# Kernel optimization log

Hardware: AMD Instinct MI355X
Metric: run time of the kernel (lower is better)

Reference implementation:

```python
import jax, jax.numpy as jnp
import numpy as np

N_HEAD = 12

def setup_inputs() -> dict:
    key = jax.random.key(0)
    ks = jax.random.split(key, 5)
    B, T, C = 4, 2048, 768
    x = jax.random.normal(ks[0], (B, T, C), dtype=jnp.float32)
    s_in = 1.0 / np.sqrt(C)
    W_qkv = jax.random.normal(ks[1], (C, 3 * C), dtype=jnp.float32) * s_in
    b_qkv = jnp.zeros((3 * C,), dtype=jnp.float32)
    W_proj = jax.random.normal(ks[2], (C, C), dtype=jnp.float32) * s_in
    b_proj = jnp.zeros((C,), dtype=jnp.float32)
    return {"x": x, "W_qkv": W_qkv, "b_qkv": b_qkv, "W_proj": W_proj, "b_proj": b_proj}


def reference(x, W_qkv, b_qkv, W_proj, b_proj):
    B, T, C = x.shape
    H = N_HEAD
    D = C // H  # head dim
    qkv = x @ W_qkv + b_qkv                      # [B,T,3C]
    q, k, v = jnp.split(qkv, 3, axis=-1)
    # [B,T,C] -> [B,H,T,D]
    q = q.reshape(B, T, H, D).transpose(0, 2, 1, 3)
    k = k.reshape(B, T, H, D).transpose(0, 2, 1, 3)
    v = v.reshape(B, T, H, D).transpose(0, 2, 1, 3)
    att = jnp.einsum("bhqd,bhkd->bhqk", q, k) / jnp.sqrt(jnp.asarray(D, x.dtype))
    causal = jnp.tril(jnp.ones((T, T), dtype=bool))
    att = jnp.where(causal, att, jnp.asarray(-jnp.inf, att.dtype))
    att = jax.nn.softmax(att, axis=-1)
    y = jnp.einsum("bhqk,bhkd->bhqd", att, v)    # [B,H,T,D]
    y = y.transpose(0, 2, 1, 3).reshape(B, T, C)
    return y @ W_proj + b_proj
```

## Files before the change

### kernel.cpp

```cpp
#include <hip/hip_runtime.h>
#include <hip/hip_bf16.h>

typedef __bf16 bf16x8 __attribute__((ext_vector_type(8)));
typedef float f32x4 __attribute__((ext_vector_type(4)));
typedef unsigned int u32x4 __attribute__((ext_vector_type(4)));
typedef unsigned int u32x2 __attribute__((ext_vector_type(2)));
typedef int i32x2 __attribute__((ext_vector_type(2)));
typedef unsigned short u16;
typedef unsigned long long u64;

#define WAITVM(n) asm volatile("s_waitcnt vmcnt(" #n ")" ::: "memory")
#define SBAR() asm volatile("s_barrier" ::: "memory")

__device__ __forceinline__ u16 f2bf(float f) {
  unsigned u = __builtin_bit_cast(unsigned, f);
  u += 0x7FFFu + ((u >> 16) & 1u);
  return (u16)(u >> 16);
}
__device__ __forceinline__ unsigned cvtpk(float a, float b) {
  float2 f; f.x = a; f.y = b;
  __hip_bfloat162 h = __float22bfloat162_rn(f);
  unsigned u;
  __builtin_memcpy(&u, &h, 4);
  return u;
}

__device__ __forceinline__ void plswap(unsigned &a, unsigned &b) {
  i32x2 r = __builtin_amdgcn_permlane32_swap((int)a, (int)b, false, false);
  a = (unsigned)r[0];
  b = (unsigned)r[1];
}

__device__ __forceinline__ void gll16(const u16* g, u16* l) {
  __builtin_amdgcn_global_load_lds(
      (const __attribute__((address_space(1))) unsigned int*)g,
      (__attribute__((address_space(3))) unsigned int*)l, 16, 0, 0);
}

__global__ void cast_x_kernel(const float* __restrict__ in, u16* __restrict__ out, int n4) {
  int i = blockIdx.x * blockDim.x + threadIdx.x;
  if (i >= n4) return;
  f32x4 v = *(const f32x4*)(in + (size_t)i * 4);
  u32x2 pk;
  pk[0] = cvtpk(v[0], v[1]);
  pk[1] = cvtpk(v[2], v[3]);
  *(u32x2*)(out + (size_t)i * 4) = pk;
}

__global__ void transpose_cast_kernel(const float* __restrict__ W, u16* __restrict__ WT, int K, int N) {
  __shared__ float tile[32][33];
  int c0 = blockIdx.x * 32, r0 = blockIdx.y * 32;
  int tx = threadIdx.x & 31, tg = threadIdx.x >> 5;
#pragma unroll
  for (int i = 0; i < 4; ++i) {
    int r = tg + i * 8;
    tile[r][tx] = W[(size_t)(r0 + r) * N + c0 + tx];
  }
  __syncthreads();
#pragma unroll
  for (int i = 0; i < 4; ++i) {
    int r = tg + i * 8;
    WT[(size_t)(c0 + r) * K + r0 + tx] = f2bf(tile[tx][r]);
  }
}

__global__ __launch_bounds__(256, 3) void gemm_qkv_kernel(
    const u16* __restrict__ A, const u16* __restrict__ BT, const float* __restrict__ bias,
    u16* __restrict__ Qb, u16* __restrict__ Kb, u16* __restrict__ Vt) {
  constexpr int K = 768;
  constexpr int NS = K / 32;
  __shared__ u16 Asm[3][128 * 32];
  __shared__ u16 Bsm[3][128 * 32];
  const int tid = threadIdx.x;
  const int w = tid >> 6, lane = tid & 63;
  const int l15 = lane & 15, quad = lane >> 4;
  const int srow = tid >> 2, scol = (tid & 3) * 8;
  const int m0 = blockIdx.y * 128, n0 = blockIdx.x * 128;
  const u16* Ag = A + (size_t)(m0 + srow) * K + scol;
  const u16* Bg = BT + (size_t)(n0 + srow) * K + scol;
  const int mw = (w >> 1) * 64, nw = (w & 1) * 64;
  f32x4 acc[4][4];
#pragma unroll
  for (int i = 0; i < 4; ++i)
#pragma unroll
    for (int j = 0; j < 4; ++j) acc[i][j] = {0.f, 0.f, 0.f, 0.f};

  auto STAGE = [&](int buf, int ks) {
    const u16* a = Ag + ks * 32;
    const u16* b = Bg + ks * 32;
#pragma unroll
    for (int rb = 0; rb < 2; ++rb) {
      gll16(a + (size_t)rb * 64 * K, &Asm[buf][(rb * 64 + w * 16) * 32]);
      gll16(b + (size_t)rb * 64 * K, &Bsm[buf][(rb * 64 + w * 16) * 32]);
    }
  };
  auto COMPUTE = [&](int buf) {
    bf16x8 af[4], bfj[4];
#pragma unroll
    for (int i = 0; i < 4; ++i) af[i] = *(const bf16x8*)&Asm[buf][(mw + i * 16 + l15) * 32 + quad * 8];
#pragma unroll
    for (int j = 0; j < 4; ++j) bfj[j] = *(const bf16x8*)&Bsm[buf][(nw + j * 16 + l15) * 32 + quad * 8];
#pragma unroll
    for (int i = 0; i < 4; ++i)
#pragma unroll
      for (int j = 0; j < 4; ++j)
        acc[i][j] = __builtin_amdgcn_mfma_f32_16x16x32_bf16(af[i], bfj[j], acc[i][j], 0, 0, 0);
  };

  STAGE(0, 0);
  STAGE(1, 1);
  for (int s = 0; s < NS - 3; s += 3) {
    STAGE((s + 2) % 3, s + 2); WAITVM(8); SBAR(); COMPUTE(s % 3); SBAR();
    STAGE((s + 3) % 3, s + 3); WAITVM(8); SBAR(); COMPUTE((s + 1) % 3); SBAR();
    STAGE((s + 4) % 3, s + 4); WAITVM(8); SBAR(); COMPUTE((s + 2) % 3); SBAR();
  }
  STAGE((NS - 1) % 3, NS - 1); WAITVM(8); SBAR(); COMPUTE((NS - 3) % 3); SBAR();
  WAITVM(4); SBAR(); COMPUTE((NS - 2) % 3); SBAR();
  WAITVM(0); SBAR(); COMPUTE((NS - 1) % 3);

  const int sec = blockIdx.x / 6;
  const int nbase = n0 - sec * 768;
#pragma unroll
  for (int j = 0; j < 4; ++j) {
    const int nloc = nbase + nw + j * 16 + l15;
    const float bv = bias[sec * 768 + nloc];
    const int h = nloc >> 6, d = nloc & 63;
#pragma unroll
    for (int i = 0; i < 4; ++i) {
      const int m = m0 + mw + i * 16 + quad * 4;
      const int bb = m >> 11, trow = m & 2047;
      if (sec == 2) {
        u32x2 pk;
        pk[0] = cvtpk(acc[i][j][0] + bv, acc[i][j][1] + bv);
        pk[1] = cvtpk(acc[i][j][2] + bv, acc[i][j][3] + bv);
        *(u32x2*)(Vt + (size_t)((bb * 12 + h) * 64 + d) * 2048 + trow) = pk;
      } else {
        u16* dst = (sec == 0) ? Qb : Kb;
        const float scl = (sec == 0) ? 0.125f * 1.44269504f : 1.0f;
#pragma unroll
        for (int r = 0; r < 4; ++r)
          dst[(size_t)((bb * 12 + h) * 2048 + trow + r) * 64 + d] = f2bf((acc[i][j][r] + bv) * scl);
      }
    }
  }
}

__global__ __launch_bounds__(256, 4) void gemm_proj_kernel(
    const u16* __restrict__ A, const u16* __restrict__ BT, const float* __restrict__ bias,
    float* __restrict__ out) {
  constexpr int K = 768;
  constexpr int NS = K / 32;
  __shared__ u16 Asm[2][64 * 32];
  __shared__ u16 Bsm[2][128 * 32];
  const int lin = blockIdx.y * 6 + blockIdx.x;
  const int swz = (lin & 7) * 96 + (lin >> 3);
  const int tid = threadIdx.x;
  const int w = tid >> 6, lane = tid & 63;
  const int l15 = lane & 15, quad = lane >> 4;
  const int srow = tid >> 2, scol = (tid & 3) * 8;
  const int m0 = (swz / 6) * 64, n0 = (swz % 6) * 128;
  const u16* Ag = A + (size_t)(m0 + srow) * K + scol;
  const u16* Bg = BT + (size_t)(n0 + srow) * K + scol;
  const int mw = (w >> 1) * 32, nw = (w & 1) * 64;
  f32x4 acc[2][4];
#pragma unroll
  for (int i = 0; i < 2; ++i)
#pragma unroll
    for (int j = 0; j < 4; ++j) acc[i][j] = {0.f, 0.f, 0.f, 0.f};

  auto STAGE = [&](int buf, int ks) {
    const u16* a = Ag + ks * 32;
    const u16* b = Bg + ks * 32;
    gll16(a, &Asm[buf][(w * 16) * 32]);
#pragma unroll
    for (int rb = 0; rb < 2; ++rb)
      gll16(b + (size_t)rb * 64 * K, &Bsm[buf][(rb * 64 + w * 16) * 32]);
  };
  auto COMPUTE = [&](int buf) {
    bf16x8 af[2], bfj[4];
#pragma unroll
    for (int i = 0; i < 2; ++i) af[i] = *(const bf16x8*)&Asm[buf][(mw + i * 16 + l15) * 32 + quad * 8];
#pragma unroll
    for (int j = 0; j < 4; ++j) bfj[j] = *(const bf16x8*)&Bsm[buf][(nw + j * 16 + l15) * 32 + quad * 8];
#pragma unroll
    for (int i = 0; i < 2; ++i)
#pragma unroll
      for (int j = 0; j < 4; ++j)
        acc[i][j] = __builtin_amdgcn_mfma_f32_16x16x32_bf16(af[i], bfj[j], acc[i][j], 0, 0, 0);
  };

  STAGE(0, 0);
  WAITVM(0); SBAR();
  for (int s = 0; s < NS; ++s) {
    const int buf = s & 1;
    if (s + 1 < NS) STAGE(buf ^ 1, s + 1);
    COMPUTE(buf);
    WAITVM(0); SBAR();
  }

#pragma unroll
  for (int j = 0; j < 4; ++j) {
    const int n = n0 + nw + j * 16 + l15;
    const float bv = bias[n];
#pragma unroll
    for (int i = 0; i < 2; ++i) {
      const int m = m0 + mw + i * 16 + quad * 4;
#pragma unroll
      for (int r = 0; r < 4; ++r) out[(size_t)(m + r) * 768 + n] = acc[i][j][r] + bv;
    }
  }
}

__global__ __launch_bounds__(512) void attn_split_kernel(
    const u16* __restrict__ Qg, const u16* __restrict__ Kg, const u16* __restrict__ Vtg,
    u16* __restrict__ Yb, float* __restrict__ Opart, float* __restrict__ lpart) {
  constexpr int T = 2048, D = 64;
  constexpr int LDP = 72;
  constexpr float MBOUND = 20.0f;
  __shared__ u16 Ks[2][64 * LDP];
  __shared__ u16 VTs[2][64 * LDP];
  const int lin = blockIdx.y * 40 + blockIdx.x;
  const int swzb = (lin & 7) * 240 + (lin >> 3);
  const int s = 39 - (swzb % 40);
  const int bh = swzb / 40;
  int qt2, c;
  if (s < 4) { qt2 = s; c = 0; }
  else if (s < 12) { qt2 = 4 + ((s - 4) >> 1); c = (s - 4) & 1; }
  else if (s < 24) { int u = s - 12; int q3 = u / 3; qt2 = 8 + q3; c = u - 3 * q3; }
  else { int u = s - 24; qt2 = 12 + (u >> 2); c = u & 3; }
  const int nkt = 2 * qt2 + 2;
  const int niter = min(8, nkt - 8 * c);
  const int tid = threadIdx.x;
  const int w = tid >> 6, lane = tid & 63;
  const int l15 = lane & 15, quad = lane >> 4;
  const int srow = tid >> 3;
  const int scol = (tid & 7) * 8;
  const int so0 = scol - 4 * (tid & 1);
  const int so1 = scol + 8 - 4 * (tid & 1);
  const u16* Kp = Kg + (size_t)bh * T * D;
  const u16* VTp = Vtg + (size_t)bh * D * T;

  const int wdiag = 2 * qt2 + (w >> 2);
  const int qq = qt2 * 128 + w * 16 + l15;
  const u16* qrow = Qg + ((size_t)bh * T + qq) * D;
  const bf16x8 qfa = *(const bf16x8*)(qrow + quad * 8);
  const bf16x8 qfb = *(const bf16x8*)(qrow + 32 + quad * 8);

  u32x4 onesw; onesw[0] = 0x3F803F80u; onesw[1] = 0x3F803F80u; onesw[2] = 0x3F803F80u; onesw[3] = 0x3F803F80u;
  const bf16x8 ones = __builtin_bit_cast(bf16x8, onesw);

  f32x4 o[4] = {{0,0,0,0},{0,0,0,0},{0,0,0,0},{0,0,0,0}};
  f32x4 lacc = {0.f, 0.f, 0.f, 0.f};

  u32x4 kA, vA;
  auto LOADT = [&](int kt) {
    const int k1 = kt * 64;
    kA = *(const u32x4*)(Kp + (size_t)(k1 + srow) * D + scol);
    vA = *(const u32x4*)(VTp + (size_t)srow * T + k1 + scol);
  };
  auto STORET = [&](int buf) {
    *(u32x4*)&Ks[buf][srow * LDP + scol] = kA;
    u32x2 vlo; vlo[0] = vA[0]; vlo[1] = vA[1];
    u32x2 vhi; vhi[0] = vA[2]; vhi[1] = vA[3];
    *(u32x2*)&VTs[buf][srow * LDP + so0] = vlo;
    *(u32x2*)&VTs[buf][srow * LDP + so1] = vhi;
  };

  LOADT(c * 8);
  STORET(0);
  if (niter > 1) LOADT(c * 8 + 1);
  __syncthreads();

  for (int j = 0; j < niter; ++j) {
    const int buf = j & 1;
    const int ktg = c * 8 + j;
    if (ktg <= wdiag) {
      f32x4 sA[4];
#pragma unroll
      for (int t = 0; t < 4; ++t) sA[t] = {-MBOUND, -MBOUND, -MBOUND, -MBOUND};
      __builtin_amdgcn_s_setprio(1);
#pragma unroll
      for (int t = 0; t < 4; ++t) {
        const bf16x8 kf0 = *(const bf16x8*)&Ks[buf][(t * 16 + l15) * LDP + quad * 8];
        const bf16x8 kf1 = *(const bf16x8*)&Ks[buf][(t * 16 + l15) * LDP + 32 + quad * 8];
        sA[t] = __builtin_amdgcn_mfma_f32_16x16x32_bf16(kf0, qfa, sA[t], 0, 0, 0);
        sA[t] = __builtin_amdgcn_mfma_f32_16x16x32_bf16(kf1, qfb, sA[t], 0, 0, 0);
      }
      __builtin_amdgcn_s_setprio(0);
      if (ktg == wdiag) {
        const int k0 = ktg * 64;
#pragma unroll
        for (int t = 0; t < 4; ++t)
#pragma unroll
          for (int r = 0; r < 4; ++r)
            if (k0 + t * 16 + quad * 4 + r > qq) sA[t][r] = -1e30f;
      }
      unsigned W[4][2];
#pragma unroll
      for (int t = 0; t < 4; ++t) {
        float e0 = __builtin_amdgcn_exp2f(sA[t][0]);
        float e1 = __builtin_amdgcn_exp2f(sA[t][1]);
        float e2 = __builtin_amdgcn_exp2f(sA[t][2]);
        float e3 = __builtin_amdgcn_exp2f(sA[t][3]);
        W[t][0] = cvtpk(e0, e1);
        W[t][1] = cvtpk(e2, e3);
      }
      plswap(W[0][0], W[1][0]);
      plswap(W[0][1], W[1][1]);
      plswap(W[2][0], W[3][0]);
      plswap(W[2][1], W[3][1]);
      u32x4 paw; paw[0] = W[0][0]; paw[1] = W[0][1]; paw[2] = W[1][0]; paw[3] = W[1][1];
      u32x4 pbw; pbw[0] = W[2][0]; pbw[1] = W[2][1]; pbw[2] = W[3][0]; pbw[3] = W[3][1];
      const bf16x8 pa = __builtin_bit_cast(bf16x8, paw);
      const bf16x8 pb = __builtin_bit_cast(bf16x8, pbw);
      __builtin_amdgcn_s_setprio(1);
      lacc = __builtin_amdgcn_mfma_f32_16x16x32_bf16(ones, pa, lacc, 0, 0, 0);
      lacc = __builtin_amdgcn_mfma_f32_16x16x32_bf16(ones, pb, lacc, 0, 0, 0);
#pragma unroll
      for (int t = 0; t < 4; ++t) {
        const bf16x8 vf0 = *(const bf16x8*)&VTs[buf][(t * 16 + l15) * LDP + quad * 8];
        const bf16x8 vf1 = *(const bf16x8*)&VTs[buf][(t * 16 + l15) * LDP + 32 + quad * 8];
        o[t] = __builtin_amdgcn_mfma_f32_16x16x32_bf16(vf0, pa, o[t], 0, 0, 0);
        o[t] = __builtin_amdgcn_mfma_f32_16x16x32_bf16(vf1, pb, o[t], 0, 0, 0);
      }
      __builtin_amdgcn_s_setprio(0);
    }
    if (j + 1 < niter) {
      STORET(buf ^ 1);
      if (j + 2 < niter) LOADT(c * 8 + j + 2);
    }
    __syncthreads();
  }

  const float lv = lacc[0];
  if (qt2 <= 3) {
    const float inv = 1.f / lv;
    const int bidx = bh / 12, hidx = bh % 12;
    u16* y = Yb + ((size_t)bidx * T + qq) * 768 + hidx * 64;
#pragma unroll
    for (int t = 0; t < 4; ++t) {
      u32x2 pk;
      pk[0] = cvtpk(o[t][0] * inv, o[t][1] * inv);
      pk[1] = cvtpk(o[t][2] * inv, o[t][3] * inv);
      *(u32x2*)(y + t * 16 + quad * 4) = pk;
    }
  } else {
    const size_t pidx = (size_t)bh * 40 + s;
    float* Op = Opart + pidx * 8192 + (size_t)(w * 16 + l15) * 64;
#pragma unroll
    for (int t = 0; t < 4; ++t) *(f32x4*)(Op + t * 16 + quad * 4) = o[t];
    if (quad == 0) lpart[pidx * 128 + w * 16 + l15] = lv;
  }
}

__global__ __launch_bounds__(256) void attn_combine_kernel(
    const float* __restrict__ Opart, const float* __restrict__ lpart, u16* __restrict__ Yb) {
  constexpr int T = 2048;
  const int qt2 = 4 + blockIdx.x;
  const int bh = blockIdx.y;
  const int nch = (qt2 < 8) ? 2 : (qt2 < 12) ? 3 : 4;
  const int off = (qt2 < 8) ? 4 + (qt2 - 4) * 2 : (qt2 < 12) ? 12 + (qt2 - 8) * 3 : 24 + (qt2 - 12) * 4;
  const size_t base = (size_t)bh * 40 + off;
  const int tid = threadIdx.x;
  const int q = tid >> 1, db = (tid & 1) * 32;
  f32x4 o[8] = {{0,0,0,0},{0,0,0,0},{0,0,0,0},{0,0,0,0},{0,0,0,0},{0,0,0,0},{0,0,0,0},{0,0,0,0}};
  float l = 0.f;
  for (int cc = 0; cc < nch; ++cc) {
    const float* Op = Opart + (base + cc) * 8192 + (size_t)q * 64 + db;
#pragma unroll
    for (int v = 0; v < 8; ++v) o[v] += *(const f32x4*)(Op + v * 4);
    l += lpart[(base + cc) * 128 + q];
  }
  const float inv = 1.f / l;
  const int bidx = bh / 12, hidx = bh % 12;
  u16* y = Yb + ((size_t)bidx * T + qt2 * 128 + q) * 768 + hidx * 64 + db;
#pragma unroll
  for (int g = 0; g < 2; ++g) {
    u32x4 pk;
    pk[0] = cvtpk(o[g * 4 + 0][0] * inv, o[g * 4 + 0][1] * inv);
    pk[1] = cvtpk(o[g * 4 + 0][2] * inv, o[g * 4 + 0][3] * inv);
    pk[2] = cvtpk(o[g * 4 + 1][0] * inv, o[g * 4 + 1][1] * inv);
    pk[3] = cvtpk(o[g * 4 + 1][2] * inv, o[g * 4 + 1][3] * inv);
    *(u32x4*)(y + g * 16) = pk;
    pk[0] = cvtpk(o[g * 4 + 2][0] * inv, o[g * 4 + 2][1] * inv);
    pk[1] = cvtpk(o[g * 4 + 2][2] * inv, o[g * 4 + 2][3] * inv);
    pk[2] = cvtpk(o[g * 4 + 3][0] * inv, o[g * 4 + 3][1] * inv);
    pk[3] = cvtpk(o[g * 4 + 3][2] * inv, o[g * 4 + 3][3] * inv);
    *(u32x4*)(y + g * 16 + 8) = pk;
  }
}

__global__ __launch_bounds__(256) void attn_kernel(
    const u16* __restrict__ Qg, const u16* __restrict__ Kg, const u16* __restrict__ Vtg,
    u16* __restrict__ Yb) {
  constexpr int T = 2048, D = 64;
  constexpr int LDP = 72;
  constexpr float MBOUND = 20.0f;
  __shared__ u16 Ks[64 * LDP];
  __shared__ u16 VTs[64 * LDP];
  __shared__ u16 Ps[4 * 32 * LDP];
  const int qb = 15 - blockIdx.x;
  const int bh = blockIdx.y;
  const int Q0 = qb * 128;
  const int bidx = bh / 12, hidx = bh % 12;
  const int tid = threadIdx.x;
  const int w = tid >> 6, lane = tid & 63;
  const int l15 = lane & 15, quad = lane >> 4;
  const int srow = tid >> 2, scol = (tid & 3) * 16;
  const u16* Kp = Kg + (size_t)bh * T * D;
  const u16* VTp = Vtg + (size_t)bh * D * T;
  u16* pw0 = &Ps[(w * 32) * LDP];
  u16* pw1 = &Ps[(w * 32 + 16) * LDP];
  const u16* qrow0 = Qg + ((size_t)bh * T + Q0 + w * 16 + l15) * D;
  const bf16x8 qf0a = *(const bf16x8*)(qrow0 + quad * 8);
  const bf16x8 qf0b = *(const bf16x8*)(qrow0 + 32 + quad * 8);
  const bf16x8 qf1a = *(const bf16x8*)(qrow0 + (size_t)64 * D + quad * 8);
  const bf16x8 qf1b = *(const bf16x8*)(qrow0 + (size_t)64 * D + 32 + quad * 8);
  const int qq0 = Q0 + w * 16 + l15, qq1 = qq0 + 64;
  f32x4 o0[4] = {{0,0,0,0},{0,0,0,0},{0,0,0,0},{0,0,0,0}};
  f32x4 o1[4] = {{0,0,0,0},{0,0,0,0},{0,0,0,0},{0,0,0,0}};
  float l0v = 0.f, l1v = 0.f;
  const int nkt = 2 * qb + 2;
  u32x4 kA = *(const u32x4*)(Kp + (size_t)srow * D + scol);
  u32x4 kB = *(const u32x4*)(Kp + (size_t)srow * D + scol + 8);
  u32x4 vA = *(const u32x4*)(VTp + (size_t)srow * T + scol);
  u32x4 vB = *(const u32x4*)(VTp + (size_t)srow * T + scol + 8);
  for (int kt = 0; kt < nkt; ++kt) {
    __syncthreads();
    *(u32x4*)&Ks[srow * LDP + scol] = kA;
    *(u32x4*)&Ks[srow * LDP + scol + 8] = kB;
    *(u32x4*)&VTs[srow * LDP + scol] = vA;
    *(u32x4*)&VTs[srow * LDP + scol + 8] = vB;
    __syncthreads();
    if (kt + 1 < nkt) {
      const int k1 = (kt + 1) * 64;
      kA = *(const u32x4*)(Kp + (size_t)(k1 + srow) * D + scol);
      kB = *(const u32x4*)(Kp + (size_t)(k1 + srow) * D + scol + 8);
      vA = *(const u32x4*)(VTp + (size_t)srow * T + k1 + scol);
      vB = *(const u32x4*)(VTp + (size_t)srow * T + k1 + scol + 8);
    }
    const int k0 = kt * 64;
    const bool g0a = (kt <= 2 * qb);
    f32x4 s0[4] = {{0,0,0,0},{0,0,0,0},{0,0,0,0},{0,0,0,0}};
    f32x4 s1[4] = {{0,0,0,0},{0,0,0,0},{0,0,0,0},{0,0,0,0}};
#pragma unroll
    for (int t = 0; t < 4; ++t) {
      const bf16x8 kf0 = *(const bf16x8*)&Ks[(t * 16 + l15) * LDP + quad * 8];
      const bf16x8 kf1 = *(const bf16x8*)&Ks[(t * 16 + l15) * LDP + 32 + quad * 8];
      s0[t] = __builtin_amdgcn_mfma_f32_16x16x32_bf16(kf0, qf0a, s0[t], 0, 0, 0);
      s0[t] = __builtin_amdgcn_mfma_f32_16x16x32_bf16(kf1, qf0b, s0[t], 0, 0, 0);
      s1[t] = __builtin_amdgcn_mfma_f32_16x16x32_bf16(kf0, qf1a, s1[t], 0, 0, 0);
      s1[t] = __builtin_amdgcn_mfma_f32_16x16x32_bf16(kf1, qf1b, s1[t], 0, 0, 0);
    }
    if (g0a) {
      if (kt == 2 * qb) {
#pragma unroll
        for (int t = 0; t < 4; ++t)
#pragma unroll
          for (int r = 0; r < 4; ++r)
            if (k0 + t * 16 + quad * 4 + r > qq0) s0[t][r] = -1e30f;
      }
#pragma unroll
      for (int t = 0; t < 4; ++t) {
        float e0 = __builtin_amdgcn_exp2f(s0[t][0] - MBOUND);
        float e1 = __builtin_amdgcn_exp2f(s0[t][1] - MBOUND);
        float e2 = __builtin_amdgcn_exp2f(s0[t][2] - MBOUND);
        float e3 = __builtin_amdgcn_exp2f(s0[t][3] - MBOUND);
        l0v += (e0 + e1) + (e2 + e3);
        u32x2 pk;
        pk[0] = cvtpk(e0, e1);
        pk[1] = cvtpk(e2, e3);
        *(u32x2*)&pw0[l15 * LDP + t * 16 + quad * 4] = pk;
      }
    }
    {
      if (kt == 2 * qb + 1) {
#pragma unroll
        for (int t = 0; t < 4; ++t)
#pragma unroll
          for (int r = 0; r < 4; ++r)
            if (k0 + t * 16 + quad * 4 + r > qq1) s1[t][r] = -1e30f;
      }
#pragma unroll
      for (int t = 0; t < 4; ++t) {
        float e0 = __builtin_amdgcn_exp2f(s1[t][0] - MBOUND);
        float e1 = __builtin_amdgcn_exp2f(s1[t][1] - MBOUND);
        float e2 = __builtin_amdgcn_exp2f(s1[t][2] - MBOUND);
        float e3 = __builtin_amdgcn_exp2f(s1[t][3] - MBOUND);
        l1v += (e0 + e1) + (e2 + e3);
        u32x2 pk;
        pk[0] = cvtpk(e0, e1);
        pk[1] = cvtpk(e2, e3);
        *(u32x2*)&pw1[l15 * LDP + t * 16 + quad * 4] = pk;
      }
    }
    const bf16x8 p0a = *(const bf16x8*)&pw0[l15 * LDP + quad * 8];
    const bf16x8 p0b = *(const bf16x8*)&pw0[l15 * LDP + 32 + quad * 8];
    const bf16x8 p1a = *(const bf16x8*)&pw1[l15 * LDP + quad * 8];
    const bf16x8 p1b = *(const bf16x8*)&pw1[l15 * LDP + 32 + quad * 8];
#pragma unroll
    for (int t = 0; t < 4; ++t) {
      const bf16x8 vf0 = *(const bf16x8*)&VTs[(t * 16 + l15) * LDP + quad * 8];
      const bf16x8 vf1 = *(const bf16x8*)&VTs[(t * 16 + l15) * LDP + 32 + quad * 8];
      if (g0a) {
        o0[t] = __builtin_amdgcn_mfma_f32_16x16x32_bf16(vf0, p0a, o0[t], 0, 0, 0);
        o0[t] = __builtin_amdgcn_mfma_f32_16x16x32_bf16(vf1, p0b, o0[t], 0, 0, 0);
      }
      o1[t] = __builtin_amdgcn_mfma_f32_16x16x32_bf16(vf0, p1a, o1[t], 0, 0, 0);
      o1[t] = __builtin_amdgcn_mfma_f32_16x16x32_bf16(vf1, p1b, o1[t], 0, 0, 0);
    }
  }
  l0v += __shfl_xor(l0v, 16); l0v += __shfl_xor(l0v, 32);
  l1v += __shfl_xor(l1v, 16); l1v += __shfl_xor(l1v, 32);
  const float inv0 = 1.f / l0v, inv1 = 1.f / l1v;
  u16* y0 = Yb + ((size_t)bidx * T + qq0) * 768 + hidx * 64;
  u16* y1 = Yb + ((size_t)bidx * T + qq1) * 768 + hidx * 64;
#pragma unroll
  for (int t = 0; t < 4; ++t) {
    u32x2 pk0, pk1;
    pk0[0] = cvtpk(o0[t][0] * inv0, o0[t][1] * inv0);
    pk0[1] = cvtpk(o0[t][2] * inv0, o0[t][3] * inv0);
    pk1[0] = cvtpk(o1[t][0] * inv1, o1[t][1] * inv1);
    pk1[1] = cvtpk(o1[t][2] * inv1, o1[t][3] * inv1);
    *(u32x2*)(y0 + t * 16 + quad * 4) = pk0;
    *(u32x2*)(y1 + t * 16 + quad * 4) = pk1;
  }
}

extern "C" void kernel_launch(void* const* d_in, const int* in_sizes, int n_in,
                              void* d_out, int out_size, void* d_ws, size_t ws_size,
                              hipStream_t stream) {
  const float* x = (const float*)d_in[0];
  const float* W_qkv = (const float*)d_in[1];
  const float* b_qkv = (const float*)d_in[2];
  const float* W_proj = (const float*)d_in[3];
  const float* b_proj = (const float*)d_in[4];
  float* out = (float*)d_out;

  constexpr size_t MC = (size_t)8192 * 768;
  u16* xb = (u16*)d_ws;
  u16* Qb = xb + MC;
  u16* Kb = Qb + MC;
  u16* Vt = Kb + MC;
  u16* Yb = Vt + MC;
  u16* WqkvT = Yb + MC;
  u16* WprojT = WqkvT + (size_t)2304 * 768;
  constexpr size_t BASE_U16 = 5 * MC + (size_t)2304 * 768 + (size_t)768 * 768;
  float* Opart = (float*)((u16*)d_ws + BASE_U16);
  float* lpart = Opart + (size_t)1920 * 8192;
  constexpr size_t NEED = BASE_U16 * 2 + ((size_t)1920 * 8192 + (size_t)1920 * 128) * 4;
  const bool use_split = (ws_size >= NEED);

  cast_x_kernel<<<6291456 / (4 * 256), 256, 0, stream>>>(x, xb, 6291456 / 4);
  transpose_cast_kernel<<<dim3(2304 / 32, 768 / 32), 256, 0, stream>>>(W_qkv, WqkvT, 768, 2304);
  transpose_cast_kernel<<<dim3(768 / 32, 768 / 32), 256, 0, stream>>>(W_proj, WprojT, 768, 768);
  gemm_qkv_kernel<<<dim3(18, 64), 256, 0, stream>>>(xb, WqkvT, b_qkv, Qb, Kb, Vt);
  if (use_split) {
    attn_split_kernel<<<dim3(40, 48), 512, 0, stream>>>(Qb, Kb, Vt, Yb, Opart, lpart);
    attn_combine_kernel<<<dim3(12, 48), 256, 0, stream>>>(Opart, lpart, Yb);
  } else {
    attn_kernel<<<dim3(16, 48), 256, 0, stream>>>(Qb, Kb, Vt, Yb);
  }
  gemm_proj_kernel<<<dim3(6, 128), 256, 0, stream>>>(Yb, WprojT, b_proj, out);
}
```

Measured before the change: 223.1 us.

## Triple-buffer proj GEMM loads and coarsen attention split-K to two chunks

The output projection GEMM moves from a double-buffered loop with a full vmcnt(0) wait every step to a three-stage LDS ring with partial waits, so two tiles of loads stay in flight while computing. The attention split scheme changes from up to four 8-tile chunks per query tile (40 blocks per head) to half-splitting only query tiles 8 and above (24 blocks per head). Tiles 0-7 now run unsplit, and the combine kernel always merges two partials. This cuts partial-sum traffic and combine work but makes blocks longer and less balanced, and the extra LDS buffer may lower occupancy of the GEMM.

Measured after the change: 217.3 us. -2.6%, faster.

```diff
diff --git a/kernel.cpp b/kernel.cpp
--- a/kernel.cpp
+++ b/kernel.cpp
@@ -150,8 +150,8 @@
     float* __restrict__ out) {
   constexpr int K = 768;
   constexpr int NS = K / 32;
-  __shared__ u16 Asm[2][64 * 32];
-  __shared__ u16 Bsm[2][128 * 32];
+  __shared__ u16 Asm[3][64 * 32];
+  __shared__ u16 Bsm[3][128 * 32];
   const int lin = blockIdx.y * 6 + blockIdx.x;
   const int swz = (lin & 7) * 96 + (lin >> 3);
   const int tid = threadIdx.x;
@@ -190,13 +190,15 @@
   };
 
   STAGE(0, 0);
-  WAITVM(0); SBAR();
-  for (int s = 0; s < NS; ++s) {
-    const int buf = s & 1;
-    if (s + 1 < NS) STAGE(buf ^ 1, s + 1);
-    COMPUTE(buf);
-    WAITVM(0); SBAR();
-  }
+  STAGE(1, 1);
+  for (int s = 0; s < NS - 3; s += 3) {
+    STAGE((s + 2) % 3, s + 2); WAITVM(6); SBAR(); COMPUTE(s % 3); SBAR();
+    STAGE((s + 3) % 3, s + 3); WAITVM(6); SBAR(); COMPUTE((s + 1) % 3); SBAR();
+    STAGE((s + 4) % 3, s + 4); WAITVM(6); SBAR(); COMPUTE((s + 2) % 3); SBAR();
+  }
+  STAGE((NS - 1) % 3, NS - 1); WAITVM(6); SBAR(); COMPUTE((NS - 3) % 3); SBAR();
+  WAITVM(3); SBAR(); COMPUTE((NS - 2) % 3); SBAR();
+  WAITVM(0); SBAR(); COMPUTE((NS - 1) % 3);
 
 #pragma unroll
   for (int j = 0; j < 4; ++j) {
@@ -219,17 +221,17 @@
   constexpr float MBOUND = 20.0f;
   __shared__ u16 Ks[2][64 * LDP];
   __shared__ u16 VTs[2][64 * LDP];
-  const int lin = blockIdx.y * 40 + blockIdx.x;
-  const int swzb = (lin & 7) * 240 + (lin >> 3);
-  const int s = 39 - (swzb % 40);
-  const int bh = swzb / 40;
+  const int lin = blockIdx.y * 24 + blockIdx.x;
+  const int swzb = (lin & 7) * 144 + (lin >> 3);
+  const int s = 23 - (swzb % 24);
+  const int bh = swzb / 24;
   int qt2, c;
-  if (s < 4) { qt2 = s; c = 0; }
-  else if (s < 12) { qt2 = 4 + ((s - 4) >> 1); c = (s - 4) & 1; }
-  else if (s < 24) { int u = s - 12; int q3 = u / 3; qt2 = 8 + q3; c = u - 3 * q3; }
-  else { int u = s - 24; qt2 = 12 + (u >> 2); c = u & 3; }
+  if (s < 8) { qt2 = s; c = 0; }
+  else { qt2 = 8 + ((s - 8) >> 1); c = (s - 8) & 1; }
   const int nkt = 2 * qt2 + 2;
-  const int niter = min(8, nkt - 8 * c);
+  const int half = nkt >> 1;
+  const int start = c ? half : 0;
+  const int niter = (qt2 < 8) ? nkt : half;
   const int tid = threadIdx.x;
   const int w = tid >> 6, lane = tid & 63;
   const int l15 = lane & 15, quad = lane >> 4;
@@ -266,14 +268,14 @@
     *(u32x2*)&VTs[buf][srow * LDP + so1] = vhi;
   };
 
-  LOADT(c * 8);
+  LOADT(start);
   STORET(0);
-  if (niter > 1) LOADT(c * 8 + 1);
+  if (niter > 1) LOADT(start + 1);
   __syncthreads();
 
   for (int j = 0; j < niter; ++j) {
     const int buf = j & 1;
-    const int ktg = c * 8 + j;
+    const int ktg = start + j;
     if (ktg <= wdiag) {
       f32x4 sA[4];
 #pragma unroll
@@ -327,13 +329,13 @@
     }
     if (j + 1 < niter) {
       STORET(buf ^ 1);
-      if (j + 2 < niter) LOADT(c * 8 + j + 2);
+      if (j + 2 < niter) LOADT(start + j + 2);
     }
     __syncthreads();
   }
 
   const float lv = lacc[0];
-  if (qt2 <= 3) {
+  if (qt2 <= 7) {
     const float inv = 1.f / lv;
     const int bidx = bh / 12, hidx = bh % 12;
     u16* y = Yb + ((size_t)bidx * T + qq) * 768 + hidx * 64;
@@ -345,7 +347,7 @@
       *(u32x2*)(y + t * 16 + quad * 4) = pk;
     }
   } else {
-    const size_t pidx = (size_t)bh * 40 + s;
+    const size_t pidx = (size_t)bh * 24 + s;
     float* Op = Opart + pidx * 8192 + (size_t)(w * 16 + l15) * 64;
 #pragma unroll
     for (int t = 0; t < 4; ++t) *(f32x4*)(Op + t * 16 + quad * 4) = o[t];
@@ -356,16 +358,14 @@
 __global__ __launch_bounds__(256) void attn_combine_kernel(
     const float* __restrict__ Opart, const float* __restrict__ lpart, u16* __restrict__ Yb) {
   constexpr int T = 2048;
-  const int qt2 = 4 + blockIdx.x;
+  const int qt2 = 8 + blockIdx.x;
   const int bh = blockIdx.y;
-  const int nch = (qt2 < 8) ? 2 : (qt2 < 12) ? 3 : 4;
-  const int off = (qt2 < 8) ? 4 + (qt2 - 4) * 2 : (qt2 < 12) ? 12 + (qt2 - 8) * 3 : 24 + (qt2 - 12) * 4;
-  const size_t base = (size_t)bh * 40 + off;
+  const size_t base = (size_t)bh * 24 + 8 + (qt2 - 8) * 2;
   const int tid = threadIdx.x;
   const int q = tid >> 1, db = (tid & 1) * 32;
   f32x4 o[8] = {{0,0,0,0},{0,0,0,0},{0,0,0,0},{0,0,0,0},{0,0,0,0},{0,0,0,0},{0,0,0,0},{0,0,0,0}};
   float l = 0.f;
-  for (int cc = 0; cc < nch; ++cc) {
+  for (int cc = 0; cc < 2; ++cc) {
     const float* Op = Opart + (base + cc) * 8192 + (size_t)q * 64 + db;
 #pragma unroll
     for (int v = 0; v < 8; ++v) o[v] += *(const f32x4*)(Op + v * 4);
@@ -556,8 +556,8 @@
   transpose_cast_kernel<<<dim3(768 / 32, 768 / 32), 256, 0, stream>>>(W_proj, WprojT, 768, 768);
   gemm_qkv_kernel<<<dim3(18, 64), 256, 0, stream>>>(xb, WqkvT, b_qkv, Qb, Kb, Vt);
   if (use_split) {
-    attn_split_kernel<<<dim3(40, 48), 512, 0, stream>>>(Qb, Kb, Vt, Yb, Opart, lpart);
-    attn_combine_kernel<<<dim3(12, 48), 256, 0, stream>>>(Opart, lpart, Yb);
+    attn_split_kernel<<<dim3(24, 48), 512, 0, stream>>>(Qb, Kb, Vt, Yb, Opart, lpart);
+    attn_combine_kernel<<<dim3(8, 48), 256, 0, stream>>>(Opart, lpart, Yb);
   } else {
     attn_kernel<<<dim3(16, 48), 256, 0, stream>>>(Qb, Kb, Vt, Yb);
   }
```
